# Kernel optimization log

Hardware: AMD Instinct MI355X
Metric: run time of the kernel (lower is better)

The kernel has to match this reference:

```python
import jax, jax.numpy as jnp
import numpy as np

NE, NR = 100000, 50
E, H, M = 512, 8, 8
HD = E // H
B = 65536


def setup_inputs() -> dict:
    key = jax.random.key(0)
    ks = jax.random.split(key, 24)
    xav = lambda k, shp: jax.random.normal(k, shp, jnp.float32) * (2.0 / (shp[0] + shp[-1])) ** 0.5
    return {
        'entity_emb': xav(ks[0], (NE, E)),
        'relation_emb': xav(ks[1], (NR, E)),
        'dens_ent_emb': jax.random.normal(ks[2], (NE, E), jnp.float32) * 0.02,
        'dens_ent_w': xav(ks[3], (E, 1)), 'dens_ent_b': jnp.zeros((1,), jnp.float32),
        'dens_rel_emb': jax.random.normal(ks[4], (NR, E), jnp.float32) * 0.02,
        'dens_rel_w': xav(ks[5], (E, 1)), 'dens_rel_b': jnp.zeros((1,), jnp.float32),
        'local_motifs': xav(ks[6], (M, HD)),
        'global_motifs': xav(ks[7], (M, HD)),
        'Wq': xav(ks[8], (E, E)), 'bq': jnp.zeros((E,), jnp.float32),
        'Wkl': xav(ks[9], (HD, HD)), 'bkl': jnp.zeros((HD,), jnp.float32),
        'Wkg': xav(ks[10], (HD, HD)), 'bkg': jnp.zeros((HD,), jnp.float32),
        'Wout': xav(ks[11], (2 * E, E)), 'bout': jnp.zeros((E,), jnp.float32),
        'adv_w': jnp.float32(1.0), 'adv_b': jnp.float32(0.0),
        'h_idx': jax.random.randint(ks[12], (B,), 0, NE),
        'r_idx': jax.random.randint(ks[13], (B,), 0, NR),
        't_idx': jax.random.randint(ks[14], (B,), 0, NE),
    }


def reference(entity_emb, relation_emb, dens_ent_emb, dens_ent_w, dens_ent_b,
              dens_rel_emb, dens_rel_w, dens_rel_b, local_motifs, global_motifs,
              Wq, bq, Wkl, bkl, Wkg, bkg, Wout, bout, adv_w, adv_b,
              h_idx, r_idx, t_idx):
    h = entity_emb[h_idx]           # [B, E]
    r = relation_emb[r_idx]
    t = entity_emb[t_idx]
    # density gating: sigmoid(Linear(Embedding(idx))) per head/tail/relation, averaged
    h_d = jax.nn.sigmoid(dens_ent_emb[h_idx] @ dens_ent_w + dens_ent_b)   # [B,1]
    t_d = jax.nn.sigmoid(dens_ent_emb[t_idx] @ dens_ent_w + dens_ent_b)
    r_d = jax.nn.sigmoid(dens_rel_emb[r_idx] @ dens_rel_w + dens_rel_b)
    density = (h_d + t_d + r_d) / 3.0                                     # [B,1]
    diff = h + r - t
    # hierarchical soft attention over local/global motif codebooks
    ctx = h + r + t
    q = (ctx @ Wq + bq).reshape(-1, H, HD)                                # [B,H,HD]
    lk = local_motifs @ Wkl + bkl                                         # [M,HD]
    gk = global_motifs @ Wkg + bkg
    scale = 1.0 / jnp.sqrt(jnp.asarray(HD, q.dtype))
    dens = density[:, :, None]                                            # [B,1,1]
    l_w = jax.nn.softmax(jnp.einsum('bhd,md->bhm', q, lk) * scale + dens, axis=-1)
    g_w = jax.nn.softmax(jnp.einsum('bhd,md->bhm', q, gk) * scale + dens, axis=-1)
    attn = (l_w + g_w) / 2.0                                              # [B,H,M]
    motifs = local_motifs + global_motifs                                 # [M,HD]
    motif_repr = jnp.einsum('bhm,md->bhd', attn, motifs).reshape(-1, E)   # [B,E]
    motif_loss = jnp.sum((diff - motif_repr) ** 2, axis=-1)               # ||.||^2
    combined = jnp.concatenate([diff, motif_repr], axis=-1)               # [B,2E]
    transformed = jnp.tanh(combined @ Wout + bout)
    score = adv_w * jnp.linalg.norm(transformed, axis=-1) + adv_b
    return score, motif_loss
```

## Files before the change

kernel.cpp:

```cpp
#include <hip/hip_runtime.h>
#include <math.h>

#define B_TOT 65536

typedef __attribute__((ext_vector_type(4))) float f32x4;
typedef __attribute__((ext_vector_type(4))) unsigned int u32x4;
typedef __attribute__((ext_vector_type(8))) __bf16 bf16x8;

#define OFF_WLOGT 0u
#define OFF_CBIAS 131072u
#define OFF_BCAT  131584u
#define OFF_MOTIF 721408u
#define OFF_LK    723456u
#define OFF_GK    725504u
#define OFF_G     727552u
#define OFF_DIFF  1048576u
#define OFF_ATTN  68157440u
#define OFF_SSQ   76546048u

__device__ __forceinline__ unsigned short f2bf(float x) {
  union { float f; unsigned int u; } v; v.f = x;
  return (unsigned short)((v.u + 0x7FFFu + ((v.u >> 16) & 1u)) >> 16);
}

__device__ __forceinline__ float bf2f(unsigned short u) {
  union { unsigned int i; float f; } v; v.i = ((unsigned int)u) << 16; return v.f;
}

__global__ __launch_bounds__(256) void k0a(
    const float* __restrict__ lm, const float* __restrict__ gm,
    const float* __restrict__ Wkl, const float* __restrict__ bkl,
    const float* __restrict__ Wkg, const float* __restrict__ bkg,
    const float* __restrict__ bq,
    float* __restrict__ lk, float* __restrict__ gk,
    float* __restrict__ motifs, float* __restrict__ G, float* __restrict__ cb) {
  int tid = threadIdx.x;
  for (int o = tid; o < 512; o += 256) {
    int m = o >> 6, d = o & 63;
    float s1 = bkl[d], s2 = bkg[d];
    for (int k = 0; k < 64; ++k) {
      s1 += lm[m*64+k] * Wkl[k*64+d];
      s2 += gm[m*64+k] * Wkg[k*64+d];
    }
    lk[o] = s1; gk[o] = s2;
    motifs[o] = lm[o] + gm[o];
  }
  __syncthreads();
  if (tid < 64) {
    int m = tid >> 3, n = tid & 7;
    float s = 0.f;
    for (int d = 0; d < 64; ++d) s += motifs[m*64+d] * motifs[n*64+d];
    G[tid] = s;
  }
  if (tid < 128) {
    int s_ = tid >> 6, h = (tid >> 3) & 7, m = tid & 7;
    const float* K = s_ ? gk : lk;
    float s = 0.f;
    for (int d = 0; d < 64; ++d) s += bq[h*64+d] * K[m*64+d];
    cb[tid] = 0.125f * s;
  }
}

__global__ __launch_bounds__(256) void k0b(
    const float* __restrict__ Wq, const float* __restrict__ Wout,
    const float* __restrict__ lk, const float* __restrict__ gk,
    const float* __restrict__ motifs,
    unsigned short* __restrict__ wlogT, unsigned short* __restrict__ bcatT) {
  int idx = blockIdx.x * 256 + threadIdx.x;
  if (idx >= 65536 + 512*576) return;
  if (idx < 65536) {
    int c = idx >> 9, k = idx & 511;
    int s_ = c >> 6, h = (c >> 3) & 7, m = c & 7;
    const float* K = (s_ ? gk : lk) + m*64;
    const float* wq = Wq + (size_t)k*512 + h*64;
    float s = 0.f;
    for (int d = 0; d < 64; ++d) s += wq[d] * K[d];
    wlogT[(size_t)c*512 + k] = f2bf(0.125f * s);
  } else {
    int i2 = idx - 65536;
    int n = i2 / 576, k = i2 - n*576;
    float v;
    if (k < 512) {
      v = Wout[(size_t)k*512 + n];
    } else {
      int hm = k - 512, h = hm >> 3, m = hm & 7;
      const float* mo = motifs + m*64;
      const float* wo = Wout + (size_t)(512 + h*64)*512 + n;
      v = 0.f;
      for (int d = 0; d < 64; ++d) v += mo[d] * wo[(size_t)d*512];
    }
    bcatT[(size_t)n*576 + k] = f2bf(v);
  }
}

__global__ __launch_bounds__(256, 4) void kA(
    const float* __restrict__ ent, const float* __restrict__ rel,
    const int* __restrict__ hI, const int* __restrict__ rI, const int* __restrict__ tI,
    const unsigned short* __restrict__ wlogT, const float* __restrict__ cb,
    unsigned short* __restrict__ diffB, unsigned short* __restrict__ attnB) {
  __shared__ __align__(16) unsigned char smem[32768];
  unsigned short* As = (unsigned short*)smem;
  unsigned short* Bs = (unsigned short*)(smem + 9216);
  float* lg  = (float*)smem;

  int tid = threadIdx.x;
  int l = tid & 63, wid = tid >> 6;
  int wr = wid >> 1, wc = wid & 1;
  int rowBase = blockIdx.x * 64;
  int r_loc = tid >> 2, p = tid & 3;
  int b = rowBase + r_loc;

  int hi = hI[b], ri = rI[b], ti = tI[b];
  const float* hp = ent + (size_t)hi * 512;
  const float* tp = ent + (size_t)ti * 512;
  const float* rp = rel + (size_t)ri * 512;
  int bn = tid >> 1, half = tid & 1;
  const unsigned short* wsrc = wlogT + (size_t)bn * 512 + half * 32;

  f32x4 acc[2][4] = {};

  float4 gh[4], gt[4], gr[4];
  u32x4 wb[4];

  {
    int q0 = p*8, q1 = 32 + p*8;
    gh[0] = *(const float4*)(hp + q0); gh[1] = *(const float4*)(hp + q0 + 4);
    gh[2] = *(const float4*)(hp + q1); gh[3] = *(const float4*)(hp + q1 + 4);
    gt[0] = *(const float4*)(tp + q0); gt[1] = *(const float4*)(tp + q0 + 4);
    gt[2] = *(const float4*)(tp + q1); gt[3] = *(const float4*)(tp + q1 + 4);
    gr[0] = *(const float4*)(rp + q0); gr[1] = *(const float4*)(rp + q0 + 4);
    gr[2] = *(const float4*)(rp + q1); gr[3] = *(const float4*)(rp + q1 + 4);
    #pragma unroll
    for (int o = 0; o < 4; ++o) wb[o] = *(const u32x4*)(wsrc + o*8);
  }

  #pragma unroll
  for (int c = 0; c < 8; ++c) {
    int k0 = c * 64;
    union { u32x4 v[2]; unsigned short s[16]; } pd, pc;
    #pragma unroll
    for (int g = 0; g < 4; ++g) {
      #pragma unroll
      for (int j = 0; j < 4; ++j) {
        float hv = ((const float*)&gh[g])[j];
        float tv = ((const float*)&gt[g])[j];
        float rv = ((const float*)&gr[g])[j];
        pd.s[g*4+j] = f2bf(hv + rv - tv);
        pc.s[g*4+j] = f2bf(hv + rv + tv);
      }
    }

    __syncthreads();
    *(u32x4*)(As + r_loc*72 + p*8)      = pc.v[0];
    *(u32x4*)(As + r_loc*72 + 32 + p*8) = pc.v[1];
    {
      unsigned short* bp = Bs + bn*72 + half*32;
      *(u32x4*)(bp)      = wb[0];
      *(u32x4*)(bp + 8)  = wb[1];
      *(u32x4*)(bp + 16) = wb[2];
      *(u32x4*)(bp + 24) = wb[3];
    }
    *(u32x4*)(diffB + (size_t)b*512 + k0 + p*8)      = pd.v[0];
    *(u32x4*)(diffB + (size_t)b*512 + k0 + 32 + p*8) = pd.v[1];
    __syncthreads();
    if (c < 7) {
      int q0 = k0 + 64 + p*8, q1 = k0 + 96 + p*8;
      gh[0] = *(const float4*)(hp + q0); gh[1] = *(const float4*)(hp + q0 + 4);
      gh[2] = *(const float4*)(hp + q1); gh[3] = *(const float4*)(hp + q1 + 4);
      gt[0] = *(const float4*)(tp + q0); gt[1] = *(const float4*)(tp + q0 + 4);
      gt[2] = *(const float4*)(tp + q1); gt[3] = *(const float4*)(tp + q1 + 4);
      gr[0] = *(const float4*)(rp + q0); gr[1] = *(const float4*)(rp + q0 + 4);
      gr[2] = *(const float4*)(rp + q1); gr[3] = *(const float4*)(rp + q1 + 4);
      #pragma unroll
      for (int o = 0; o < 4; ++o) wb[o] = *(const u32x4*)(wsrc + (c+1)*64 + o*8);
    }
    #pragma unroll
    for (int kf = 0; kf < 2; ++kf) {
      bf16x8 af0 = *(const bf16x8*)(As + (wr*32 +      (l & 15))*72 + kf*32 + 8*(l >> 4));
      bf16x8 af1 = *(const bf16x8*)(As + (wr*32 + 16 + (l & 15))*72 + kf*32 + 8*(l >> 4));
      #pragma unroll
      for (int n = 0; n < 4; ++n) {
        bf16x8 bfr = *(const bf16x8*)(Bs + (wc*64 + n*16 + (l & 15))*72 + kf*32 + 8*(l >> 4));
        acc[0][n] = __builtin_amdgcn_mfma_f32_16x16x32_bf16(af0, bfr, acc[0][n], 0, 0, 0);
        acc[1][n] = __builtin_amdgcn_mfma_f32_16x16x32_bf16(af1, bfr, acc[1][n], 0, 0, 0);
      }
    }
  }

  __syncthreads();
  #pragma unroll
  for (int m = 0; m < 2; ++m)
    #pragma unroll
    for (int n = 0; n < 4; ++n)
      #pragma unroll
      for (int j = 0; j < 4; ++j) {
        int rr = wr*32 + m*16 + 4*(l >> 4) + j;
        int cc = wc*64 + n*16 + (l & 15);
        lg[rr*128 + ((cc + rr) & 127)] = acc[m][n][j];
      }
  __syncthreads();

  #pragma unroll
  for (int e = 0; e < 2; ++e) {
    int h = 2*p + e;
    float a8[8];
    #pragma unroll
    for (int m = 0; m < 8; ++m) a8[m] = 0.f;
    #pragma unroll
    for (int s = 0; s < 2; ++s) {
      float v[8], mx = -1e30f;
      #pragma unroll
      for (int m = 0; m < 8; ++m) {
        int cc = s*64 + h*8 + m;
        v[m] = lg[r_loc*128 + ((cc + r_loc) & 127)] + cb[cc];
        mx = fmaxf(mx, v[m]);
      }
      float sum = 0.f;
      #pragma unroll
      for (int m = 0; m < 8; ++m) { v[m] = __expf(v[m] - mx); sum += v[m]; }
      float inv = 0.5f / sum;
      #pragma unroll
      for (int m = 0; m < 8; ++m) a8[m] += v[m] * inv;
    }
    union { u32x4 v; unsigned short s[8]; } pk;
    #pragma unroll
    for (int m = 0; m < 8; ++m) pk.s[m] = f2bf(a8[m]);
    *(u32x4*)(attnB + (size_t)b*64 + h*8) = pk.v;
  }
}

__global__ __launch_bounds__(256) void kC(
    const unsigned short* __restrict__ diffB, const unsigned short* __restrict__ attnB,
    const float* __restrict__ motifs, float* __restrict__ lossOut) {
  __shared__ float mo[512];
  int tid = threadIdx.x;
  mo[tid] = motifs[tid];
  mo[tid + 256] = motifs[tid + 256];
  __syncthreads();
  int l = tid & 63;
  int b = blockIdx.x * 4 + (tid >> 6);
  union { u32x4 v; unsigned short s[8]; } dv, av;
  dv.v = *(const u32x4*)(diffB + (size_t)b*512 + l*8);
  int h = l >> 3;
  av.v = *(const u32x4*)(attnB + (size_t)b*64 + h*8);
  float at[8], df[8];
  #pragma unroll
  for (int j = 0; j < 8; ++j) { df[j] = bf2f(dv.s[j]); at[j] = bf2f(av.s[j]); }
  int dbase = (l & 7) * 8;
  float part = 0.f;
  #pragma unroll
  for (int j = 0; j < 8; ++j) {
    float repr = 0.f;
    #pragma unroll
    for (int m = 0; m < 8; ++m) repr += at[m] * mo[m*64 + dbase + j];
    float e = df[j] - repr;
    part += e * e;
  }
  #pragma unroll
  for (int off = 1; off < 64; off <<= 1) part += __shfl_xor(part, off, 64);
  if (l == 0) lossOut[b] = part;
}

__global__ __launch_bounds__(512, 4) void kB(
    const unsigned short* __restrict__ diffB, const unsigned short* __restrict__ attnB,
    const unsigned short* __restrict__ bcatT, const float* __restrict__ bout,
    float* __restrict__ ssqPart) {
  __shared__ __align__(16) unsigned short As[128*40];
  __shared__ __align__(16) unsigned short Bs[256*40];
  __shared__ float part[128*4];
  int tid = threadIdx.x;
  int l = tid & 63, wid = tid >> 6;
  int wr = wid >> 2, wc = wid & 3;
  int mblk = blockIdx.x >> 1, nblk = blockIdx.x & 1;
  int rowBase = mblk * 128;
  int colBase = nblk * 256;
  f32x4 acc[4][4] = {};
  int ar = tid >> 2, aq = tid & 3;
  int bn2 = tid >> 1, half = tid & 1;
  int bx2 = (bn2 >> 3) & 3;

  u32x4 na, nb0, nb1;
  {
    na = *(const u32x4*)(diffB + (size_t)(rowBase + ar)*512 + aq*8);
    const u32x4* src = (const u32x4*)(bcatT + (size_t)(colBase + bn2)*576 + half*16);
    nb0 = src[0]; nb1 = src[1];
  }
  for (int ks = 0; ks < 18; ++ks) {
    __syncthreads();
    *(u32x4*)(&As[ar*40 + aq*8]) = na;
    {
      unsigned short* bp = &Bs[bn2*40];
      int j0 = half*2, j1 = half*2 + 1;
      *(u32x4*)(bp + (j0^bx2)*8) = nb0;
      *(u32x4*)(bp + (j1^bx2)*8) = nb1;
    }
    __syncthreads();
    if (ks < 17) {
      int k0 = (ks + 1) * 32;
      const unsigned short* srcp = (k0 < 512)
        ? diffB + (size_t)(rowBase + ar)*512 + k0 + aq*8
        : attnB + (size_t)(rowBase + ar)*64 + (k0 - 512) + aq*8;
      na = *(const u32x4*)srcp;
      const u32x4* src = (const u32x4*)(bcatT + (size_t)(colBase + bn2)*576 + k0 + half*16);
      nb0 = src[0]; nb1 = src[1];
    }
    {
      bf16x8 af[4];
      #pragma unroll
      for (int m = 0; m < 4; ++m)
        af[m] = *(const bf16x8*)(&As[(wr*64 + m*16 + (l & 15))*40 + 8*(l >> 4)]);
      #pragma unroll
      for (int n = 0; n < 4; ++n) {
        int col = wc*64 + n*16 + (l & 15);
        int g = (l >> 4) ^ ((col >> 3) & 3);
        bf16x8 bfr = *(const bf16x8*)(&Bs[col*40 + g*8]);
        #pragma unroll
        for (int m = 0; m < 4; ++m)
          acc[m][n] = __builtin_amdgcn_mfma_f32_16x16x32_bf16(af[m], bfr, acc[m][n], 0, 0, 0);
      }
    }
  }
  __syncthreads();
  float bo[4];
  #pragma unroll
  for (int n = 0; n < 4; ++n) bo[n] = bout[colBase + wc*64 + n*16 + (l & 15)];
  #pragma unroll
  for (int m = 0; m < 4; ++m) {
    float ss0 = 0.f, ss1 = 0.f, ss2 = 0.f, ss3 = 0.f;
    #pragma unroll
    for (int n = 0; n < 4; ++n) {
      float t0 = tanhf(acc[m][n][0] + bo[n]); ss0 += t0*t0;
      float t1 = tanhf(acc[m][n][1] + bo[n]); ss1 += t1*t1;
      float t2 = tanhf(acc[m][n][2] + bo[n]); ss2 += t2*t2;
      float t3 = tanhf(acc[m][n][3] + bo[n]); ss3 += t3*t3;
    }
    #pragma unroll
    for (int mask = 1; mask < 16; mask <<= 1) {
      ss0 += __shfl_xor(ss0, mask, 64);
      ss1 += __shfl_xor(ss1, mask, 64);
      ss2 += __shfl_xor(ss2, mask, 64);
      ss3 += __shfl_xor(ss3, mask, 64);
    }
    if ((l & 15) == 0) {
      int rbase = wr*64 + m*16 + (l >> 4)*4;
      part[(rbase+0)*4 + wc] = ss0;
      part[(rbase+1)*4 + wc] = ss1;
      part[(rbase+2)*4 + wc] = ss2;
      part[(rbase+3)*4 + wc] = ss3;
    }
  }
  __syncthreads();
  if (tid < 128) {
    float s = part[tid*4] + part[tid*4+1] + part[tid*4+2] + part[tid*4+3];
    ssqPart[(size_t)nblk*B_TOT + rowBase + tid] = s;
  }
}

__global__ __launch_bounds__(256) void kD(
    const float* __restrict__ ssqPart, const float* __restrict__ advw,
    const float* __restrict__ advb, float* __restrict__ scoreOut) {
  int i = blockIdx.x * 256 + threadIdx.x;
  float s = ssqPart[i] + ssqPart[B_TOT + i];
  scoreOut[i] = advw[0] * sqrtf(s) + advb[0];
}

extern "C" void kernel_launch(void* const* d_in, const int* in_sizes, int n_in,
                              void* d_out, int out_size, void* d_ws, size_t ws_size,
                              hipStream_t stream) {
  const float* ent  = (const float*)d_in[0];
  const float* rel  = (const float*)d_in[1];
  const float* lm   = (const float*)d_in[8];
  const float* gm   = (const float*)d_in[9];
  const float* Wq   = (const float*)d_in[10];
  const float* bq   = (const float*)d_in[11];
  const float* Wkl  = (const float*)d_in[12];
  const float* bkl  = (const float*)d_in[13];
  const float* Wkg  = (const float*)d_in[14];
  const float* bkg  = (const float*)d_in[15];
  const float* Wout = (const float*)d_in[16];
  const float* bout = (const float*)d_in[17];
  const float* advw = (const float*)d_in[18];
  const float* advb = (const float*)d_in[19];
  const int* hI = (const int*)d_in[20];
  const int* rI = (const int*)d_in[21];
  const int* tI = (const int*)d_in[22];
  char* ws = (char*)d_ws;
  unsigned short* wlogT = (unsigned short*)(ws + OFF_WLOGT);
  float* cb     = (float*)(ws + OFF_CBIAS);
  unsigned short* bcatT = (unsigned short*)(ws + OFF_BCAT);
  float* motifs = (float*)(ws + OFF_MOTIF);
  float* lk     = (float*)(ws + OFF_LK);
  float* gk     = (float*)(ws + OFF_GK);
  float* G      = (float*)(ws + OFF_G);
  unsigned short* diffB = (unsigned short*)(ws + OFF_DIFF);
  unsigned short* attnB = (unsigned short*)(ws + OFF_ATTN);
  float* ssqPart = (float*)(ws + OFF_SSQ);
  float* scoreOut = (float*)d_out;
  float* lossOut  = (float*)d_out + B_TOT;

  hipLaunchKernelGGL(k0a, dim3(1), dim3(256), 0, stream,
                     lm, gm, Wkl, bkl, Wkg, bkg, bq, lk, gk, motifs, G, cb);
  hipLaunchKernelGGL(k0b, dim3(1408), dim3(256), 0, stream,
                     Wq, Wout, lk, gk, motifs, wlogT, bcatT);
  hipLaunchKernelGGL(kA, dim3(B_TOT/64), dim3(256), 0, stream,
                     ent, rel, hI, rI, tI, wlogT, cb, diffB, attnB);
  hipLaunchKernelGGL(kC, dim3(B_TOT/4), dim3(256), 0, stream,
                     diffB, attnB, motifs, lossOut);
  hipLaunchKernelGGL(kB, dim3(B_TOT/128 * 2), dim3(512), 0, stream,
                     diffB, attnB, bcatT, bout, ssqPart);
  hipLaunchKernelGGL(kD, dim3(B_TOT/256), dim3(256), 0, stream,
                     ssqPart, advw, advb, scoreOut);
}
```

Measured before the change: 158.7 us.

## Merge setup kernels, double-buffer GEMM LDS, fuse loss and score kernels

Three changes. First, the two setup kernels become one: every block recomputes the small motif key projections into shared memory, which removes a launch and a global round trip but repeats a 512x64 matmul in each of 1408 blocks. Second, the output GEMM now double-buffers its A/B shared-memory tiles, so each k-step needs one barrier instead of two. Third, the motif-loss kernel is merged with the final score kernel to save a launch. Dropping the unused G matrix removes dead work.

Result: slower. 168.5 us (+6.2%).

```diff
diff --git a/kernel.cpp b/kernel.cpp
--- a/kernel.cpp
+++ b/kernel.cpp
@@ -11,9 +11,6 @@
 #define OFF_CBIAS 131072u
 #define OFF_BCAT  131584u
 #define OFF_MOTIF 721408u
-#define OFF_LK    723456u
-#define OFF_GK    725504u
-#define OFF_G     727552u
 #define OFF_DIFF  1048576u
 #define OFF_ATTN  68157440u
 #define OFF_SSQ   76546048u
@@ -27,13 +24,15 @@
   union { unsigned int i; float f; } v; v.i = ((unsigned int)u) << 16; return v.f;
 }
 
-__global__ __launch_bounds__(256) void k0a(
+__global__ __launch_bounds__(256) void k0(
     const float* __restrict__ lm, const float* __restrict__ gm,
     const float* __restrict__ Wkl, const float* __restrict__ bkl,
     const float* __restrict__ Wkg, const float* __restrict__ bkg,
     const float* __restrict__ bq,
-    float* __restrict__ lk, float* __restrict__ gk,
-    float* __restrict__ motifs, float* __restrict__ G, float* __restrict__ cb) {
+    const float* __restrict__ Wq, const float* __restrict__ Wout,
+    float* __restrict__ motifsG, float* __restrict__ cb,
+    unsigned short* __restrict__ wlogT, unsigned short* __restrict__ bcatT) {
+  __shared__ float lkS[512], gkS[512], moS[512];
   int tid = threadIdx.x;
   for (int o = tid; o < 512; o += 256) {
     int m = o >> 6, d = o & 63;
@@ -42,36 +41,26 @@
       s1 += lm[m*64+k] * Wkl[k*64+d];
       s2 += gm[m*64+k] * Wkg[k*64+d];
     }
-    lk[o] = s1; gk[o] = s2;
-    motifs[o] = lm[o] + gm[o];
-  }
-  __syncthreads();
-  if (tid < 64) {
-    int m = tid >> 3, n = tid & 7;
-    float s = 0.f;
-    for (int d = 0; d < 64; ++d) s += motifs[m*64+d] * motifs[n*64+d];
-    G[tid] = s;
-  }
-  if (tid < 128) {
-    int s_ = tid >> 6, h = (tid >> 3) & 7, m = tid & 7;
-    const float* K = s_ ? gk : lk;
-    float s = 0.f;
-    for (int d = 0; d < 64; ++d) s += bq[h*64+d] * K[m*64+d];
-    cb[tid] = 0.125f * s;
-  }
-}
-
-__global__ __launch_bounds__(256) void k0b(
-    const float* __restrict__ Wq, const float* __restrict__ Wout,
-    const float* __restrict__ lk, const float* __restrict__ gk,
-    const float* __restrict__ motifs,
-    unsigned short* __restrict__ wlogT, unsigned short* __restrict__ bcatT) {
-  int idx = blockIdx.x * 256 + threadIdx.x;
-  if (idx >= 65536 + 512*576) return;
+    lkS[o] = s1; gkS[o] = s2;
+    moS[o] = lm[o] + gm[o];
+  }
+  __syncthreads();
+  if (blockIdx.x == 0) {
+    if (tid < 128) {
+      int s_ = tid >> 6, h = (tid >> 3) & 7, m = tid & 7;
+      const float* K = (s_ ? gkS : lkS) + m*64;
+      float s = 0.f;
+      for (int d = 0; d < 64; ++d) s += bq[h*64+d] * K[d];
+      cb[tid] = 0.125f * s;
+    }
+    motifsG[tid] = moS[tid];
+    motifsG[tid + 256] = moS[tid + 256];
+  }
+  int idx = blockIdx.x * 256 + tid;
   if (idx < 65536) {
     int c = idx >> 9, k = idx & 511;
     int s_ = c >> 6, h = (c >> 3) & 7, m = c & 7;
-    const float* K = (s_ ? gk : lk) + m*64;
+    const float* K = (s_ ? gkS : lkS) + m*64;
     const float* wq = Wq + (size_t)k*512 + h*64;
     float s = 0.f;
     for (int d = 0; d < 64; ++d) s += wq[d] * K[d];
@@ -84,7 +73,7 @@
       v = Wout[(size_t)k*512 + n];
     } else {
       int hm = k - 512, h = hm >> 3, m = hm & 7;
-      const float* mo = motifs + m*64;
+      const float* mo = moS + m*64;
       const float* wo = Wout + (size_t)(512 + h*64)*512 + n;
       v = 0.f;
       for (int d = 0; d < 64; ++d) v += mo[d] * wo[(size_t)d*512];
@@ -229,44 +218,12 @@
   }
 }
 
-__global__ __launch_bounds__(256) void kC(
-    const unsigned short* __restrict__ diffB, const unsigned short* __restrict__ attnB,
-    const float* __restrict__ motifs, float* __restrict__ lossOut) {
-  __shared__ float mo[512];
-  int tid = threadIdx.x;
-  mo[tid] = motifs[tid];
-  mo[tid + 256] = motifs[tid + 256];
-  __syncthreads();
-  int l = tid & 63;
-  int b = blockIdx.x * 4 + (tid >> 6);
-  union { u32x4 v; unsigned short s[8]; } dv, av;
-  dv.v = *(const u32x4*)(diffB + (size_t)b*512 + l*8);
-  int h = l >> 3;
-  av.v = *(const u32x4*)(attnB + (size_t)b*64 + h*8);
-  float at[8], df[8];
-  #pragma unroll
-  for (int j = 0; j < 8; ++j) { df[j] = bf2f(dv.s[j]); at[j] = bf2f(av.s[j]); }
-  int dbase = (l & 7) * 8;
-  float part = 0.f;
-  #pragma unroll
-  for (int j = 0; j < 8; ++j) {
-    float repr = 0.f;
-    #pragma unroll
-    for (int m = 0; m < 8; ++m) repr += at[m] * mo[m*64 + dbase + j];
-    float e = df[j] - repr;
-    part += e * e;
-  }
-  #pragma unroll
-  for (int off = 1; off < 64; off <<= 1) part += __shfl_xor(part, off, 64);
-  if (l == 0) lossOut[b] = part;
-}
-
 __global__ __launch_bounds__(512, 4) void kB(
     const unsigned short* __restrict__ diffB, const unsigned short* __restrict__ attnB,
     const unsigned short* __restrict__ bcatT, const float* __restrict__ bout,
     float* __restrict__ ssqPart) {
-  __shared__ __align__(16) unsigned short As[128*40];
-  __shared__ __align__(16) unsigned short Bs[256*40];
+  __shared__ __align__(16) unsigned short As[2][128*40];
+  __shared__ __align__(16) unsigned short Bs[2][256*40];
   __shared__ float part[128*4];
   int tid = threadIdx.x;
   int l = tid & 63, wid = tid >> 6;
@@ -284,16 +241,14 @@
     na = *(const u32x4*)(diffB + (size_t)(rowBase + ar)*512 + aq*8);
     const u32x4* src = (const u32x4*)(bcatT + (size_t)(colBase + bn2)*576 + half*16);
     nb0 = src[0]; nb1 = src[1];
-  }
+    *(u32x4*)(&As[0][ar*40 + aq*8]) = na;
+    unsigned short* bp = &Bs[0][bn2*40];
+    int j0 = half*2, j1 = half*2 + 1;
+    *(u32x4*)(bp + (j0^bx2)*8) = nb0;
+    *(u32x4*)(bp + (j1^bx2)*8) = nb1;
+  }
+  int cur = 0;
   for (int ks = 0; ks < 18; ++ks) {
-    __syncthreads();
-    *(u32x4*)(&As[ar*40 + aq*8]) = na;
-    {
-      unsigned short* bp = &Bs[bn2*40];
-      int j0 = half*2, j1 = half*2 + 1;
-      *(u32x4*)(bp + (j0^bx2)*8) = nb0;
-      *(u32x4*)(bp + (j1^bx2)*8) = nb1;
-    }
     __syncthreads();
     if (ks < 17) {
       int k0 = (ks + 1) * 32;
@@ -308,17 +263,25 @@
       bf16x8 af[4];
       #pragma unroll
       for (int m = 0; m < 4; ++m)
-        af[m] = *(const bf16x8*)(&As[(wr*64 + m*16 + (l & 15))*40 + 8*(l >> 4)]);
+        af[m] = *(const bf16x8*)(&As[cur][(wr*64 + m*16 + (l & 15))*40 + 8*(l >> 4)]);
       #pragma unroll
       for (int n = 0; n < 4; ++n) {
         int col = wc*64 + n*16 + (l & 15);
         int g = (l >> 4) ^ ((col >> 3) & 3);
-        bf16x8 bfr = *(const bf16x8*)(&Bs[col*40 + g*8]);
+        bf16x8 bfr = *(const bf16x8*)(&Bs[cur][col*40 + g*8]);
         #pragma unroll
         for (int m = 0; m < 4; ++m)
           acc[m][n] = __builtin_amdgcn_mfma_f32_16x16x32_bf16(af[m], bfr, acc[m][n], 0, 0, 0);
       }
     }
+    if (ks < 17) {
+      *(u32x4*)(&As[cur^1][ar*40 + aq*8]) = na;
+      unsigned short* bp = &Bs[cur^1][bn2*40];
+      int j0 = half*2, j1 = half*2 + 1;
+      *(u32x4*)(bp + (j0^bx2)*8) = nb0;
+      *(u32x4*)(bp + (j1^bx2)*8) = nb1;
+    }
+    cur ^= 1;
   }
   __syncthreads();
   float bo[4];
@@ -356,12 +319,43 @@
   }
 }
 
-__global__ __launch_bounds__(256) void kD(
-    const float* __restrict__ ssqPart, const float* __restrict__ advw,
-    const float* __restrict__ advb, float* __restrict__ scoreOut) {
-  int i = blockIdx.x * 256 + threadIdx.x;
-  float s = ssqPart[i] + ssqPart[B_TOT + i];
-  scoreOut[i] = advw[0] * sqrtf(s) + advb[0];
+__global__ __launch_bounds__(256) void kCD(
+    const unsigned short* __restrict__ diffB, const unsigned short* __restrict__ attnB,
+    const float* __restrict__ motifs, const float* __restrict__ ssqPart,
+    const float* __restrict__ advw, const float* __restrict__ advb,
+    float* __restrict__ lossOut, float* __restrict__ scoreOut) {
+  __shared__ float mo[512];
+  int tid = threadIdx.x;
+  mo[tid] = motifs[tid];
+  mo[tid + 256] = motifs[tid + 256];
+  __syncthreads();
+  int l = tid & 63;
+  int b = blockIdx.x * 4 + (tid >> 6);
+  union { u32x4 v; unsigned short s[8]; } dv, av;
+  dv.v = *(const u32x4*)(diffB + (size_t)b*512 + l*8);
+  int h = l >> 3;
+  av.v = *(const u32x4*)(attnB + (size_t)b*64 + h*8);
+  float at[8], df[8];
+  #pragma unroll
+  for (int j = 0; j < 8; ++j) { df[j] = bf2f(dv.s[j]); at[j] = bf2f(av.s[j]); }
+  int dbase = (l & 7) * 8;
+  float part = 0.f;
+  #pragma unroll
+  for (int j = 0; j < 8; ++j) {
+    float repr = 0.f;
+    #pragma unroll
+    for (int m = 0; m < 8; ++m) repr += at[m] * mo[m*64 + dbase + j];
+    float e = df[j] - repr;
+    part += e * e;
+  }
+  #pragma unroll
+  for (int off = 1; off < 64; off <<= 1) part += __shfl_xor(part, off, 64);
+  if (l == 0) lossOut[b] = part;
+  if (tid < 4) {
+    int rb = blockIdx.x * 4 + tid;
+    float s = ssqPart[rb] + ssqPart[B_TOT + rb];
+    scoreOut[rb] = advw[0] * sqrtf(s) + advb[0];
+  }
 }
 
 extern "C" void kernel_launch(void* const* d_in, const int* in_sizes, int n_in,
@@ -389,25 +383,19 @@
   float* cb     = (float*)(ws + OFF_CBIAS);
   unsigned short* bcatT = (unsigned short*)(ws + OFF_BCAT);
   float* motifs = (float*)(ws + OFF_MOTIF);
-  float* lk     = (float*)(ws + OFF_LK);
-  float* gk     = (float*)(ws + OFF_GK);
-  float* G      = (float*)(ws + OFF_G);
   unsigned short* diffB = (unsigned short*)(ws + OFF_DIFF);
   unsigned short* attnB = (unsigned short*)(ws + OFF_ATTN);
   float* ssqPart = (float*)(ws + OFF_SSQ);
   float* scoreOut = (float*)d_out;
   float* lossOut  = (float*)d_out + B_TOT;
 
-  hipLaunchKernelGGL(k0a, dim3(1), dim3(256), 0, stream,
-                     lm, gm, Wkl, bkl, Wkg, bkg, bq, lk, gk, motifs, G, cb);
-  hipLaunchKernelGGL(k0b, dim3(1408), dim3(256), 0, stream,
-                     Wq, Wout, lk, gk, motifs, wlogT, bcatT);
+  hipLaunchKernelGGL(k0, dim3(1408), dim3(256), 0, stream,
+                     lm, gm, Wkl, bkl, Wkg, bkg, bq, Wq, Wout,
+                     motifs, cb, wlogT, bcatT);
   hipLaunchKernelGGL(kA, dim3(B_TOT/64), dim3(256), 0, stream,
                      ent, rel, hI, rI, tI, wlogT, cb, diffB, attnB);
-  hipLaunchKernelGGL(kC, dim3(B_TOT/4), dim3(256), 0, stream,
-                     diffB, attnB, motifs, lossOut);
   hipLaunchKernelGGL(kB, dim3(B_TOT/128 * 2), dim3(512), 0, stream,
                      diffB, attnB, bcatT, bout, ssqPart);
-  hipLaunchKernelGGL(kD, dim3(B_TOT/256), dim3(256), 0, stream,
-                     ssqPart, advw, advb, scoreOut);
-}
+  hipLaunchKernelGGL(kCD, dim3(B_TOT/4), dim3(256), 0, stream,
+                     diffB, attnB, motifs, ssqPart, advw, advb, lossOut, scoreOut);
+}
```
